# Kernel tuning notes

Hardware: AMD Instinct MI355X
Metric: run time of the kernel (lower is better)

## Reference

```python
import jax, jax.numpy as jnp
import numpy as np

N_NODES = 50000
N_EDGES = 800000
IN_CH = 128
HEADS = 4
OUT_CH = 32  # heads * out = in (needed for residual add)


def setup_inputs() -> dict:
    key = jax.random.key(0)
    k1, k2, k3, k4, k5, k6 = jax.random.split(key, 6)
    x = jax.random.normal(k1, (N_NODES, IN_CH), dtype=jnp.float32)
    edge_index = jax.random.randint(k2, (2, N_EDGES), 0, N_NODES, dtype=jnp.int64)
    # GATConv params: lin weight [in, heads*out], attention vectors split src/dst, bias [heads*out]
    W = jax.random.normal(k3, (IN_CH, HEADS * OUT_CH), dtype=jnp.float32) * (1.0 / np.sqrt(IN_CH))
    a_src = jax.random.normal(k4, (HEADS, OUT_CH), dtype=jnp.float32) * 0.1
    a_dst = jax.random.normal(k5, (HEADS, OUT_CH), dtype=jnp.float32) * 0.1
    bias = jax.random.normal(k6, (HEADS * OUT_CH,), dtype=jnp.float32) * 0.01
    return {"x": x, "edge_index": edge_index, "W": W, "a_src": a_src, "a_dst": a_dst, "bias": bias}


def reference(x, edge_index, W, a_src, a_dst, bias):
    N = x.shape[0]
    H, C = a_src.shape
    # PyG GATConv default: add self loops (message flows src -> dst)
    loops = jnp.arange(N, dtype=edge_index.dtype)
    src = jnp.concatenate([edge_index[0], loops])
    dst = jnp.concatenate([edge_index[1], loops])

    h = (x @ W).reshape(N, H, C)                       # [N,H,C]
    alpha_s = jnp.einsum('nhc,hc->nh', h, a_src)       # [N,H]
    alpha_d = jnp.einsum('nhc,hc->nh', h, a_dst)       # [N,H]

    # per-edge logits, LeakyReLU(0.2)
    e = jax.nn.leaky_relu(alpha_s[src] + alpha_d[dst], negative_slope=0.2)  # [E,H]
    # segment softmax over incoming edges of each destination node
    m = jax.ops.segment_max(e, dst, num_segments=N)    # [N,H]
    p = jnp.exp(e - m[dst])
    denom = jax.ops.segment_sum(p, dst, num_segments=N)
    alpha = p / (denom[dst] + 1e-16)                   # [E,H]

    # weighted scatter-sum of source features
    msg = alpha[:, :, None] * h[src]                   # [E,H,C]
    out = jax.ops.segment_sum(msg, dst, num_segments=N)
    out = out.reshape(N, H * C) + bias                 # concat heads + bias

    return jax.nn.elu(out) + x                         # ELU + residual
```

## Files before the change

### kernel.cpp

```cpp
#include <hip/hip_runtime.h>
#include <math.h>


#define CH 128
#define BCOLS 144
#define BKT_SH 8
#define BKT_CAP 8192

typedef short bf16x8 __attribute__((ext_vector_type(8)));
typedef float f32x4 __attribute__((ext_vector_type(4)));

__device__ __forceinline__ short f2bf(float f) {
    unsigned int u = __builtin_bit_cast(unsigned int, f);
    u += 0x7FFFu + ((u >> 16) & 1u);
    return (short)(u >> 16);
}
__device__ __forceinline__ unsigned int cvtpk(float lo, float hi) {
    unsigned int r;
    asm("v_cvt_pk_bf16_f32 %0, %1, %2" : "=v"(r) : "v"(lo), "v"(hi));
    return r;
}
__device__ __forceinline__ float bflo(unsigned int u) {
    return __builtin_bit_cast(float, u << 16);
}
__device__ __forceinline__ float bfhi(unsigned int u) {
    return __builtin_bit_cast(float, u & 0xffff0000u);
}

__global__ void prep(const float* __restrict__ W, const float* __restrict__ a_src,
                     const float* __restrict__ a_dst, short* __restrict__ Wbf,
                     int* __restrict__ gcursor, int nbuk) {
    int i = blockIdx.x * 256 + threadIdx.x;
    if (i < CH * CH) {
        int k = i >> 7, n = i & 127;
        Wbf[n * CH + k] = f2bf(W[i]);
    }
    if (i < 2048) {
        int k = i & 127, idx = i >> 7;
        float sum = 0.f;
        if (idx < 8) {
            int h = idx & 3;
            const float* av = (idx < 4) ? a_src : a_dst;
            #pragma unroll
            for (int c = 0; c < 32; ++c) sum += W[k * CH + h * 32 + c] * av[h * 32 + c];
        }
        Wbf[(CH + idx) * CH + k] = f2bf(sum);
    }
    if (i < nbuk) gcursor[i] = i * BKT_CAP;
}

__global__ __launch_bounds__(256) void gemm_mfma(
    const float* __restrict__ x, const short* __restrict__ Wbf,
    unsigned short* __restrict__ hb, float* __restrict__ as_, float* __restrict__ ad_,
    int N)
{
    __shared__ short Wl[BCOLS * CH];
    for (int v = threadIdx.x; v < BCOLS * 16; v += 256) {
        int n = v >> 4, k8 = v & 15;
        *(bf16x8*)&Wl[n * CH + ((k8 ^ (n & 7)) << 3)] = *(const bf16x8*)&Wbf[v * 8];
    }
    const int w = threadIdx.x >> 6, l = threadIdx.x & 63;
    const int lr = l & 15, lg = l >> 4;
    const int base = blockIdx.x * 128 + w * 32;
    __syncthreads();

    bf16x8 afr[2][4];
    #pragma unroll
    for (int mt = 0; mt < 2; ++mt) {
        int arow = base + mt * 16 + lr;
        if (arow >= N) arow = N - 1;
        const float* xr = &x[(size_t)arow * CH + lg * 8];
        #pragma unroll
        for (int ks = 0; ks < 4; ++ks) {
            float4 p0 = *(const float4*)&xr[ks * 32];
            float4 p1 = *(const float4*)&xr[ks * 32 + 4];
            uint4 aw;
            aw.x = cvtpk(p0.x, p0.y); aw.y = cvtpk(p0.z, p0.w);
            aw.z = cvtpk(p1.x, p1.y); aw.w = cvtpk(p1.z, p1.w);
            afr[mt][ks] = __builtin_bit_cast(bf16x8, aw);
        }
    }

    f32x4 acc[2][9];
    #pragma unroll
    for (int mt = 0; mt < 2; ++mt)
        #pragma unroll
        for (int nt = 0; nt < 9; ++nt) acc[mt][nt] = (f32x4){0.f, 0.f, 0.f, 0.f};

    #pragma unroll
    for (int ks = 0; ks < 4; ++ks) {
        #pragma unroll
        for (int nt = 0; nt < 9; ++nt) {
            int col = nt * 16 + lr;
            bf16x8 bfr = *(const bf16x8*)&Wl[col * CH + (((ks * 4 + lg) ^ (col & 7)) << 3)];
            acc[0][nt] = __builtin_amdgcn_mfma_f32_16x16x32_bf16(afr[0][ks], bfr, acc[0][nt], 0, 0, 0);
            acc[1][nt] = __builtin_amdgcn_mfma_f32_16x16x32_bf16(afr[1][ks], bfr, acc[1][nt], 0, 0, 0);
        }
    }

    #pragma unroll
    for (int mt = 0; mt < 2; ++mt) {
        const int rbase = base + mt * 16 + lg * 4;
        #pragma unroll
        for (int nt = 0; nt < 8; ++nt) {
            #pragma unroll
            for (int r = 0; r < 4; r += 2) {
                unsigned int u = cvtpk(acc[mt][nt][r], acc[mt][nt][r + 1]);
                int orow = rbase + r;
                if (orow < N)     hb[(size_t)orow * CH + nt * 16 + lr] = (unsigned short)u;
                if (orow + 1 < N) hb[(size_t)(orow + 1) * CH + nt * 16 + lr] = (unsigned short)(u >> 16);
            }
        }
        #pragma unroll
        for (int r = 0; r < 4; ++r) {
            int orow = rbase + r;
            float val = acc[mt][8][r];
            if (orow < N) {
                if (lr < 4)      as_[orow * 4 + lr] = val;
                else if (lr < 8) ad_[orow * 4 + lr - 4] = val;
            }
        }
    }
}

__global__ __launch_bounds__(256) void bucket_scatter(
    const int* __restrict__ src, const int* __restrict__ dst,
    int* __restrict__ gcursor, int* __restrict__ ebuf, int E, int N, int NBUK)
{
    __shared__ int lh[256], gbase[256];
    const int t = threadIdx.x;
    for (int j = t; j < NBUK; j += 256) lh[j] = 0;
    __syncthreads();
    const int total = E + N;
    const int base = blockIdx.x * 1024;
    int pv[4], bk[4], rk[4];
    #pragma unroll
    for (int k = 0; k < 4; ++k) {
        int i = base + k * 256 + t;
        if (i < total) {
            int s, d;
            if (i < E) { s = src[i]; d = dst[i]; }
            else       { s = i - E;  d = s; }
            bk[k] = d >> BKT_SH;
            pv[k] = s | ((d & 255) << 16);
            rk[k] = atomicAdd(&lh[bk[k]], 1);
        } else bk[k] = -1;
    }
    __syncthreads();
    for (int j = t; j < NBUK; j += 256)
        gbase[j] = lh[j] ? atomicAdd(&gcursor[j], lh[j]) : 0;
    __syncthreads();
    #pragma unroll
    for (int k = 0; k < 4; ++k)
        if (bk[k] >= 0) {
            int pos = gbase[bk[k]] + rk[k];
            if (pos < (bk[k] + 1) * BKT_CAP) ebuf[pos] = pv[k];
        }
}

__global__ __launch_bounds__(256) void fine_scatter(
    const int* __restrict__ gcursor, int* __restrict__ ebuf,
    int* __restrict__ row_start, int* __restrict__ row_cnt, int N)
{
    __shared__ int st[BKT_CAP];
    __shared__ int lh[256], lofs[256], lcur[256];
    __shared__ int ws[4];
    const int b = blockIdx.x, t = threadIdx.x;
    const int p0 = b * BKT_CAP;
    int cnt = gcursor[b] - p0; if (cnt > BKT_CAP) cnt = BKT_CAP;
    const int nb = b << BKT_SH;
    lh[t] = 0; lcur[t] = 0;
    __syncthreads();
    for (int e = t; e < cnt; e += 256) {
        int v = ebuf[p0 + e];
        st[e] = v;
        atomicAdd(&lh[v >> 16], 1);
    }
    __syncthreads();
    int v = lh[t], s = v;
    const int lane = t & 63, w = t >> 6;
    #pragma unroll
    for (int off = 1; off < 64; off <<= 1) {
        int u = __shfl_up(s, off, 64);
        if (lane >= off) s += u;
    }
    if (lane == 63) ws[w] = s;
    __syncthreads();
    int wadd = 0;
    if (w > 0) wadd += ws[0];
    if (w > 1) wadd += ws[1];
    if (w > 2) wadd += ws[2];
    int ex = s - v + wadd;
    lofs[t] = ex;
    if (nb + t < N) { row_start[nb + t] = p0 + ex; row_cnt[nb + t] = v; }
    __syncthreads();
    for (int e = t; e < cnt; e += 256) {
        int pv = st[e];
        int ld = pv >> 16;
        int pos = p0 + lofs[ld] + atomicAdd(&lcur[ld], 1);
        ebuf[pos] = pv & 0xFFFF;
    }
}

__global__ __launch_bounds__(256) void gat_aggregate(
    const unsigned short* __restrict__ hb, const float* __restrict__ as_,
    const float* __restrict__ ad_, const int* __restrict__ row_start,
    const int* __restrict__ row_cnt, const int* __restrict__ esrc,
    const float* __restrict__ bias, const float* __restrict__ x,
    float* __restrict__ out, int N)
{
    __shared__ float p_s[4][64];
    __shared__ int   s_s[4][16];
    int wv = threadIdx.x >> 6;
    int wid = blockIdx.x * 4 + wv;
    int lane = threadIdx.x & 63;
    if (wid >= N) return;
    const int l31 = lane & 31;
    const int half = lane >> 5;
    const int hq = lane & 3;
    const int eslot = lane >> 2;
    const int h2 = l31 >> 3;
    const float adv = ad_[wid * 4 + hq];
    const int jb = row_start[wid];
    const int je = jb + row_cnt[wid];

    float denp = 0.f;
    float acc0 = 0.f, acc1 = 0.f, acc2 = 0.f, acc3 = 0.f;
    for (int j0 = jb; j0 < je; j0 += 16) {
        int eidx = j0 + eslot;
        int s = 0; float p = 0.f;
        if (eidx < je) {
            s = esrc[eidx];
            float e = as_[s * 4 + hq] + adv;
            e = fmaxf(e, 0.2f * e);
            p = __expf(e);
        }
        p_s[wv][lane] = p;
        if (hq == 0) s_s[wv][eslot] = s;
        denp += p;
        int rem = je - j0; if (rem > 16) rem = 16;
        int npair = (rem + 1) >> 1;
        int i = 0;
        for (; i + 1 < npair; i += 2) {
            int e0 = 2 * i + half, e1 = 2 * (i + 1) + half;
            float pb0 = p_s[wv][e0 * 4 + h2];
            int   sb0 = s_s[wv][e0];
            float pb1 = p_s[wv][e1 * 4 + h2];
            int   sb1 = s_s[wv][e1];
            uint2 hv0 = *(const uint2*)&hb[(size_t)sb0 * CH + l31 * 4];
            uint2 hv1 = *(const uint2*)&hb[(size_t)sb1 * CH + l31 * 4];
            acc0 = fmaf(pb0, bflo(hv0.x), acc0);
            acc1 = fmaf(pb0, bfhi(hv0.x), acc1);
            acc2 = fmaf(pb0, bflo(hv0.y), acc2);
            acc3 = fmaf(pb0, bfhi(hv0.y), acc3);
            acc0 = fmaf(pb1, bflo(hv1.x), acc0);
            acc1 = fmaf(pb1, bfhi(hv1.x), acc1);
            acc2 = fmaf(pb1, bflo(hv1.y), acc2);
            acc3 = fmaf(pb1, bfhi(hv1.y), acc3);
        }
        if (i < npair) {
            int e0 = 2 * i + half;
            float pb0 = p_s[wv][e0 * 4 + h2];
            int   sb0 = s_s[wv][e0];
            uint2 hv0 = *(const uint2*)&hb[(size_t)sb0 * CH + l31 * 4];
            acc0 = fmaf(pb0, bflo(hv0.x), acc0);
            acc1 = fmaf(pb0, bfhi(hv0.x), acc1);
            acc2 = fmaf(pb0, bflo(hv0.y), acc2);
            acc3 = fmaf(pb0, bfhi(hv0.y), acc3);
        }
    }
    #pragma unroll
    for (int m = 4; m < 64; m <<= 1) denp += __shfl_xor(denp, m, 64);
    float den = __shfl(denp, h2, 64);
    acc0 += __shfl_xor(acc0, 32, 64);
    acc1 += __shfl_xor(acc1, 32, 64);
    acc2 += __shfl_xor(acc2, 32, 64);
    acc3 += __shfl_xor(acc3, 32, 64);
    if (half == 0) {
        float inv = 1.f / (den + 1e-16f);
        float4 bv = *(const float4*)&bias[l31 * 4];
        float4 xv = *(const float4*)&x[(size_t)wid * CH + l31 * 4];
        float o0 = acc0 * inv + bv.x;
        float o1 = acc1 * inv + bv.y;
        float o2 = acc2 * inv + bv.z;
        float o3 = acc3 * inv + bv.w;
        o0 = (o0 > 0.f) ? o0 : expm1f(o0);
        o1 = (o1 > 0.f) ? o1 : expm1f(o1);
        o2 = (o2 > 0.f) ? o2 : expm1f(o2);
        o3 = (o3 > 0.f) ? o3 : expm1f(o3);
        float4 ov = make_float4(o0 + xv.x, o1 + xv.y, o2 + xv.z, o3 + xv.w);
        *(float4*)&out[(size_t)wid * CH + l31 * 4] = ov;
    }
}

extern "C" void kernel_launch(void* const* d_in, const int* in_sizes, int n_in,
                              void* d_out, int out_size, void* d_ws, size_t ws_size,
                              hipStream_t stream) {
    const float* x     = (const float*)d_in[0];
    const int*   ei    = (const int*)d_in[1];
    const float* W     = (const float*)d_in[2];
    const float* a_src = (const float*)d_in[3];
    const float* a_dst = (const float*)d_in[4];
    const float* bias  = (const float*)d_in[5];
    float* out = (float*)d_out;

    const int N = in_sizes[0] / CH;
    const int E = in_sizes[1] / 2;
    const int* src = ei;
    const int* dst = ei + E;
    const int total = E + N;
    const int NBUK = (N + 255) >> BKT_SH;

    unsigned short* hb = (unsigned short*)d_ws;
    float* as_ = (float*)(hb + (size_t)N * CH);
    float* ad_ = as_ + (size_t)N * 4;
    short* Wbf = (short*)(ad_ + (size_t)N * 4);
    int* row_start = (int*)(Wbf + BCOLS * CH);
    int* row_cnt   = row_start + N;
    int* gcursor   = row_cnt + N;
    int* ebuf      = gcursor + 256;

    prep<<<64, 256, 0, stream>>>(W, a_src, a_dst, Wbf, gcursor, NBUK);
    gemm_mfma<<<(N + 127) / 128, 256, 0, stream>>>(x, Wbf, hb, as_, ad_, N);
    bucket_scatter<<<(total + 1023) / 1024, 256, 0, stream>>>(src, dst, gcursor, ebuf, E, N, NBUK);
    fine_scatter<<<NBUK, 256, 0, stream>>>(gcursor, ebuf, row_start, row_cnt, N);
    gat_aggregate<<<(N + 3) / 4, 256, 0, stream>>>(hb, as_, ad_, row_start, row_cnt, ebuf, bias, x, out, N);
}
```

Measured before the change: 178.5 us.

## Merge GEMM and bucket scatter into one launch; shuffle-based aggregation

The GEMM and the coarse edge-bucketing kernels become a single launch that splits blocks by index, so the two independent stages can run side by side and one launch is saved. The aggregation kernel now processes 32 edges per iteration, broadcasts probabilities and source indices with wave shuffles instead of going through shared memory, and issues four gathered row loads at a time for more memory-level parallelism. The risks are that the scatter blocks now reserve the GEMM's large shared buffer, which lowers their occupancy, and that the aggregation loop uses more registers.

```diff
diff --git a/kernel.cpp b/kernel.cpp
--- a/kernel.cpp
+++ b/kernel.cpp
@@ -49,19 +49,18 @@
     if (i < nbuk) gcursor[i] = i * BKT_CAP;
 }
 
-__global__ __launch_bounds__(256) void gemm_mfma(
-    const float* __restrict__ x, const short* __restrict__ Wbf,
+__device__ __forceinline__ void gemm_body(
+    int bid, const float* __restrict__ x, const short* __restrict__ Wbf,
     unsigned short* __restrict__ hb, float* __restrict__ as_, float* __restrict__ ad_,
-    int N)
-{
-    __shared__ short Wl[BCOLS * CH];
+    int N, short* Wl)
+{
     for (int v = threadIdx.x; v < BCOLS * 16; v += 256) {
         int n = v >> 4, k8 = v & 15;
         *(bf16x8*)&Wl[n * CH + ((k8 ^ (n & 7)) << 3)] = *(const bf16x8*)&Wbf[v * 8];
     }
     const int w = threadIdx.x >> 6, l = threadIdx.x & 63;
     const int lr = l & 15, lg = l >> 4;
-    const int base = blockIdx.x * 128 + w * 32;
+    const int base = bid * 128 + w * 32;
     __syncthreads();
 
     bf16x8 afr[2][4];
@@ -123,16 +122,16 @@
     }
 }
 
-__global__ __launch_bounds__(256) void bucket_scatter(
-    const int* __restrict__ src, const int* __restrict__ dst,
-    int* __restrict__ gcursor, int* __restrict__ ebuf, int E, int N, int NBUK)
-{
-    __shared__ int lh[256], gbase[256];
+__device__ __forceinline__ void scatter_body(
+    int bid, const int* __restrict__ src, const int* __restrict__ dst,
+    int* __restrict__ gcursor, int* __restrict__ ebuf, int E, int N, int NBUK,
+    int* lh, int* gbase)
+{
     const int t = threadIdx.x;
     for (int j = t; j < NBUK; j += 256) lh[j] = 0;
     __syncthreads();
     const int total = E + N;
-    const int base = blockIdx.x * 1024;
+    const int base = bid * 1024;
     int pv[4], bk[4], rk[4];
     #pragma unroll
     for (int k = 0; k < 4; ++k) {
@@ -158,6 +157,23 @@
         }
 }
 
+__global__ __launch_bounds__(256) void gemm_scatter(
+    const float* __restrict__ x, const short* __restrict__ Wbf,
+    unsigned short* __restrict__ hb, float* __restrict__ as_, float* __restrict__ ad_,
+    const int* __restrict__ src, const int* __restrict__ dst,
+    int* __restrict__ gcursor, int* __restrict__ ebuf,
+    int E, int N, int NBUK, int GB)
+{
+    __shared__ short Wl[BCOLS * CH];
+    if ((int)blockIdx.x < GB) {
+        gemm_body(blockIdx.x, x, Wbf, hb, as_, ad_, N, Wl);
+    } else {
+        int* lh = (int*)Wl;
+        int* gbase = lh + 256;
+        scatter_body(blockIdx.x - GB, src, dst, gcursor, ebuf, E, N, NBUK, lh, gbase);
+    }
+}
+
 __global__ __launch_bounds__(256) void fine_scatter(
     const int* __restrict__ gcursor, int* __restrict__ ebuf,
     int* __restrict__ row_start, int* __restrict__ row_cnt, int N)
@@ -202,6 +218,42 @@
     }
 }
 
+#define PAIR4(PP, SS, IBASE)                                                    \
+    {                                                                           \
+        int b0 = 8 * (IBASE) + 4 * half;                                        \
+        int b1 = b0 + 8, b2 = b0 + 16, b3 = b0 + 24;                            \
+        float pb0 = __shfl((PP), b0 + h2, 64);                                  \
+        float pb1 = __shfl((PP), b1 + h2, 64);                                  \
+        float pb2 = __shfl((PP), b2 + h2, 64);                                  \
+        float pb3 = __shfl((PP), b3 + h2, 64);                                  \
+        int sb0 = __shfl((SS), b0, 64);                                         \
+        int sb1 = __shfl((SS), b1, 64);                                         \
+        int sb2 = __shfl((SS), b2, 64);                                         \
+        int sb3 = __shfl((SS), b3, 64);                                         \
+        uint2 hv0 = *(const uint2*)&hb[(size_t)sb0 * CH + l31 * 4];             \
+        uint2 hv1 = *(const uint2*)&hb[(size_t)sb1 * CH + l31 * 4];             \
+        uint2 hv2 = *(const uint2*)&hb[(size_t)sb2 * CH + l31 * 4];             \
+        uint2 hv3 = *(const uint2*)&hb[(size_t)sb3 * CH + l31 * 4];             \
+        acc0 = fmaf(pb0, bflo(hv0.x), acc0); acc1 = fmaf(pb0, bfhi(hv0.x), acc1); \
+        acc2 = fmaf(pb0, bflo(hv0.y), acc2); acc3 = fmaf(pb0, bfhi(hv0.y), acc3); \
+        acc0 = fmaf(pb1, bflo(hv1.x), acc0); acc1 = fmaf(pb1, bfhi(hv1.x), acc1); \
+        acc2 = fmaf(pb1, bflo(hv1.y), acc2); acc3 = fmaf(pb1, bfhi(hv1.y), acc3); \
+        acc0 = fmaf(pb2, bflo(hv2.x), acc0); acc1 = fmaf(pb2, bfhi(hv2.x), acc1); \
+        acc2 = fmaf(pb2, bflo(hv2.y), acc2); acc3 = fmaf(pb2, bfhi(hv2.y), acc3); \
+        acc0 = fmaf(pb3, bflo(hv3.x), acc0); acc1 = fmaf(pb3, bfhi(hv3.x), acc1); \
+        acc2 = fmaf(pb3, bflo(hv3.y), acc2); acc3 = fmaf(pb3, bfhi(hv3.y), acc3); \
+    }
+
+#define PAIR1(PP, SS, IBASE)                                                    \
+    {                                                                           \
+        int b0 = 8 * (IBASE) + 4 * half;                                        \
+        float pb0 = __shfl((PP), b0 + h2, 64);                                  \
+        int   sb0 = __shfl((SS), b0, 64);                                       \
+        uint2 hv0 = *(const uint2*)&hb[(size_t)sb0 * CH + l31 * 4];             \
+        acc0 = fmaf(pb0, bflo(hv0.x), acc0); acc1 = fmaf(pb0, bfhi(hv0.x), acc1); \
+        acc2 = fmaf(pb0, bflo(hv0.y), acc2); acc3 = fmaf(pb0, bfhi(hv0.y), acc3); \
+    }
+
 __global__ __launch_bounds__(256) void gat_aggregate(
     const unsigned short* __restrict__ hb, const float* __restrict__ as_,
     const float* __restrict__ ad_, const int* __restrict__ row_start,
@@ -209,10 +261,7 @@
     const float* __restrict__ bias, const float* __restrict__ x,
     float* __restrict__ out, int N)
 {
-    __shared__ float p_s[4][64];
-    __shared__ int   s_s[4][16];
-    int wv = threadIdx.x >> 6;
-    int wid = blockIdx.x * 4 + wv;
+    int wid = blockIdx.x * 4 + (threadIdx.x >> 6);
     int lane = threadIdx.x & 63;
     if (wid >= N) return;
     const int l31 = lane & 31;
@@ -226,47 +275,33 @@
 
     float denp = 0.f;
     float acc0 = 0.f, acc1 = 0.f, acc2 = 0.f, acc3 = 0.f;
-    for (int j0 = jb; j0 < je; j0 += 16) {
-        int eidx = j0 + eslot;
-        int s = 0; float p = 0.f;
-        if (eidx < je) {
-            s = esrc[eidx];
-            float e = as_[s * 4 + hq] + adv;
+    for (int j0 = jb; j0 < je; j0 += 32) {
+        int ei0 = j0 + eslot, ei1 = j0 + 16 + eslot;
+        int s0 = 0, s1 = 0; float p0 = 0.f, p1 = 0.f;
+        if (ei0 < je) {
+            s0 = esrc[ei0];
+            float e = as_[s0 * 4 + hq] + adv;
             e = fmaxf(e, 0.2f * e);
-            p = __expf(e);
-        }
-        p_s[wv][lane] = p;
-        if (hq == 0) s_s[wv][eslot] = s;
-        denp += p;
-        int rem = je - j0; if (rem > 16) rem = 16;
+            p0 = __expf(e);
+        }
+        if (ei1 < je) {
+            s1 = esrc[ei1];
+            float e = as_[s1 * 4 + hq] + adv;
+            e = fmaxf(e, 0.2f * e);
+            p1 = __expf(e);
+        }
+        denp += p0 + p1;
+        int rem = je - j0; if (rem > 32) rem = 32;
         int npair = (rem + 1) >> 1;
+        int npA = npair < 8 ? npair : 8;
         int i = 0;
-        for (; i + 1 < npair; i += 2) {
-            int e0 = 2 * i + half, e1 = 2 * (i + 1) + half;
-            float pb0 = p_s[wv][e0 * 4 + h2];
-            int   sb0 = s_s[wv][e0];
-            float pb1 = p_s[wv][e1 * 4 + h2];
-            int   sb1 = s_s[wv][e1];
-            uint2 hv0 = *(const uint2*)&hb[(size_t)sb0 * CH + l31 * 4];
-            uint2 hv1 = *(const uint2*)&hb[(size_t)sb1 * CH + l31 * 4];
-            acc0 = fmaf(pb0, bflo(hv0.x), acc0);
-            acc1 = fmaf(pb0, bfhi(hv0.x), acc1);
-            acc2 = fmaf(pb0, bflo(hv0.y), acc2);
-            acc3 = fmaf(pb0, bfhi(hv0.y), acc3);
-            acc0 = fmaf(pb1, bflo(hv1.x), acc0);
-            acc1 = fmaf(pb1, bfhi(hv1.x), acc1);
-            acc2 = fmaf(pb1, bflo(hv1.y), acc2);
-            acc3 = fmaf(pb1, bfhi(hv1.y), acc3);
-        }
-        if (i < npair) {
-            int e0 = 2 * i + half;
-            float pb0 = p_s[wv][e0 * 4 + h2];
-            int   sb0 = s_s[wv][e0];
-            uint2 hv0 = *(const uint2*)&hb[(size_t)sb0 * CH + l31 * 4];
-            acc0 = fmaf(pb0, bflo(hv0.x), acc0);
-            acc1 = fmaf(pb0, bfhi(hv0.x), acc1);
-            acc2 = fmaf(pb0, bflo(hv0.y), acc2);
-            acc3 = fmaf(pb0, bfhi(hv0.y), acc3);
+        for (; i + 3 < npA; i += 4) PAIR4(p0, s0, i);
+        for (; i < npA; ++i)        PAIR1(p0, s0, i);
+        if (npair > 8) {
+            int npB = npair - 8;
+            i = 0;
+            for (; i + 3 < npB; i += 4) PAIR4(p1, s1, i);
+            for (; i < npB; ++i)        PAIR1(p1, s1, i);
         }
     }
     #pragma unroll
@@ -320,9 +355,13 @@
     int* gcursor   = row_cnt + N;
     int* ebuf      = gcursor + 256;
 
+    const int GB = (N + 127) / 128;
+    const int SB = (total + 1023) / 1024;
+
     prep<<<64, 256, 0, stream>>>(W, a_src, a_dst, Wbf, gcursor, NBUK);
-    gemm_mfma<<<(N + 127) / 128, 256, 0, stream>>>(x, Wbf, hb, as_, ad_, N);
-    bucket_scatter<<<(total + 1023) / 1024, 256, 0, stream>>>(src, dst, gcursor, ebuf, E, N, NBUK);
+    gemm_scatter<<<GB + SB, 256, 0, stream>>>(x, Wbf, hb, as_, ad_,
+                                              src, dst, gcursor, ebuf,
+                                              E, N, NBUK, GB);
     fine_scatter<<<NBUK, 256, 0, stream>>>(gcursor, ebuf, row_start, row_cnt, N);
     gat_aggregate<<<(N + 3) / 4, 256, 0, stream>>>(hb, as_, ad_, row_start, row_cnt, ebuf, bias, x, out, N);
 }
```

After: 161.9 us. -9.3%, faster.
